# Kernel tuning notes

Measured on AMD Instinct MI355X. Metric: run time of the kernel, lower is better.

Reference implementation:

```python
import jax, jax.numpy as jnp
import numpy as np

DROPOUT_P = 0.5
SCALE = float(np.sqrt(128.0))  # sqrt(dk)


def setup_inputs() -> dict:
    key = jax.random.key(0)
    kq, kk, kv = jax.random.split(key, 3)
    B, H, S, D = 2, 16, 2048, 128
    return {
        "query": jax.random.normal(kq, (B, H, S, D), dtype=jnp.float32),
        "key": jax.random.normal(kk, (B, H, S, D), dtype=jnp.float32),
        "value": jax.random.normal(kv, (B, H, S, D), dtype=jnp.float32),
    }


def reference(query, key, value):
    # qk = Q @ K^T / scale  -> [B, H, Sq, Skv]
    scores = jnp.einsum("bhqd,bhkd->bhqk", query, key) / SCALE
    probs = jax.nn.softmax(scores, axis=-1)
    # dropout with inverted scaling (torch F.dropout semantics), fixed RNG key
    keep = jax.random.bernoulli(jax.random.key(42), 1.0 - DROPOUT_P, probs.shape)
    dropped = jnp.where(keep, probs / (1.0 - DROPOUT_P), 0.0)
    # output = dropped @ V  -> [B, H, Sq, Dv]
    return jnp.einsum("bhqk,bhkd->bhqd", dropped, value)
```

## Files before the change

### kernel.cpp

```cpp
#include <hip/hip_runtime.h>
#include <cstdint>

typedef __bf16 bf16x8 __attribute__((ext_vector_type(8)));
typedef __bf16 bf16x4 __attribute__((ext_vector_type(4)));
typedef __bf16 bf16x2 __attribute__((ext_vector_type(2)));
typedef float  f32x4  __attribute__((ext_vector_type(4)));

static constexpr int Hn = 16, Sn = 2048, Dn = 128;
static constexpr float SCALE_INV = 0.088388347648318447f;
static constexpr float M0 = 4.0f;

static constexpr size_t WS_KV = 8388608;
static constexpr size_t WS_NEED = 2 * WS_KV * 2;

__device__ __forceinline__ uint32_t rotl32(uint32_t v, int s) {
  return (v << s) | (v >> (32 - s));
}

__device__ __forceinline__ void tf2x32(uint32_t c0, uint32_t c1,
                                       uint32_t& o0, uint32_t& o1) {
  const uint32_t K1 = 42u, K2 = 0x1BD11BF0u;
  uint32_t x0 = c0, x1 = c1 + K1;
#define TF_R4(a,b,c,d) \
  x0 += x1; x1 = rotl32(x1,a) ^ x0; \
  x0 += x1; x1 = rotl32(x1,b) ^ x0; \
  x0 += x1; x1 = rotl32(x1,c) ^ x0; \
  x0 += x1; x1 = rotl32(x1,d) ^ x0;
  TF_R4(13,15,26,6)   x0 += K1;            x1 += K2 + 1u;
  TF_R4(17,29,16,24)  x0 += K2;            x1 += 2u;
  TF_R4(13,15,26,6)               x1 += K1 + 3u;
  TF_R4(17,29,16,24)  x0 += K1;            x1 += K2 + 4u;
  TF_R4(13,15,26,6)   x0 += K2;            x1 += 5u;
#undef TF_R4
  o0 = x0; o1 = x1;
}

__device__ __forceinline__ bf16x8 cvt8(f32x4 a, f32x4 b) {
  bf16x8 r;
  r[0] = (__bf16)a[0]; r[1] = (__bf16)a[1]; r[2] = (__bf16)a[2]; r[3] = (__bf16)a[3];
  r[4] = (__bf16)b[0]; r[5] = (__bf16)b[1]; r[6] = (__bf16)b[2]; r[7] = (__bf16)b[3];
  return r;
}

__global__ __launch_bounds__(256) void prep_cast(
    const float* __restrict__ K, const float* __restrict__ V,
    __bf16* __restrict__ Kb, __bf16* __restrict__ Vt)
{
  int bid = (int)blockIdx.x;
  if (bid < 4096) {
    size_t base = ((size_t)bid * 256 + threadIdx.x) * 8;
    f32x4 a = *(const f32x4*)(K + base);
    f32x4 b = *(const f32x4*)(K + base + 4);
    *(bf16x8*)(Kb + base) = cvt8(a, b);
  } else {
    bid -= 4096;
    int bh = bid >> 8, kvt = (bid >> 2) & 63, dt = bid & 3;
    __shared__ float tile[32][33];
    int r = (int)threadIdx.x >> 3, c4 = ((int)threadIdx.x & 7) * 4;
    const float* Vb = V + ((size_t)bh * Sn + (size_t)kvt * 32 + r) * Dn + dt * 32 + c4;
    f32x4 v = *(const f32x4*)Vb;
    tile[r][c4] = v[0]; tile[r][c4 + 1] = v[1];
    tile[r][c4 + 2] = v[2]; tile[r][c4 + 3] = v[3];
    __syncthreads();
    bf16x4 o;
    o[0] = (__bf16)tile[c4][r];     o[1] = (__bf16)tile[c4 + 1][r];
    o[2] = (__bf16)tile[c4 + 2][r]; o[3] = (__bf16)tile[c4 + 3][r];
    __bf16* dst = Vt + ((size_t)bh * Dn + dt * 32 + r) * Sn + (size_t)kvt * 32 + c4;
    *(bf16x4*)dst = o;
  }
}

__global__ __launch_bounds__(256, 4) void attn_bf16(
    const float* __restrict__ Qg, const __bf16* __restrict__ Kb,
    const __bf16* __restrict__ Vt, float* __restrict__ Og)
{
  const int tid  = threadIdx.x;
  const int lane = tid & 63;
  const int wv   = tid >> 6;
  const int g    = lane >> 4;
  const int qp   = lane & 15;

  const int bid = (int)blockIdx.x;
  const int qt  = bid & 31;
  const int bh  = bid >> 5;
  const uint32_t b_hi = (uint32_t)(bh >> 4) << 26;
  const uint32_t h_hi = (uint32_t)(bh & 15) << 22;

  const int q0 = qt * 64 + wv * 16;

  const size_t bhOff = (size_t)bh * Sn * Dn;
  const float*  Qb  = Qg + bhOff;
  const __bf16* Kbh = Kb + bhOff;
  const __bf16* Vbh = Vt + bhOff;
  float*        Ob  = Og + bhOff;

  bf16x8 qf[4];
  {
    const float* qrow = Qb + (size_t)(q0 + qp) * Dn + g * 8;
    #pragma unroll
    for (int c = 0; c < 4; ++c) {
      f32x4 a = *(const f32x4*)(qrow + c * 32);
      f32x4 b = *(const f32x4*)(qrow + c * 32 + 4);
      #pragma unroll
      for (int j = 0; j < 4; ++j) { a[j] *= SCALE_INV; b[j] *= SCALE_INV; }
      qf[c] = cvt8(a, b);
    }
  }

  f32x4 oacc[8];
  #pragma unroll
  for (int n = 0; n < 8; ++n) { f32x4 z = {0.f,0.f,0.f,0.f}; oacc[n] = z; }
  float l_run = 0.f;

  const uint32_t idx_base = b_hi + h_hi + ((uint32_t)(q0 + qp) << 11);

  for (int kv0 = 0; kv0 < Sn; kv0 += 32) {
    f32x4 st0 = {0.f,0.f,0.f,0.f}, st1 = {0.f,0.f,0.f,0.f};
    {
      const __bf16* kr0 = Kbh + (size_t)(kv0 + qp) * Dn + g * 8;
      const __bf16* kr1 = kr0 + (size_t)16 * Dn;
      #pragma unroll
      for (int c = 0; c < 4; ++c) {
        bf16x8 ka = *(const bf16x8*)(kr0 + c * 32);
        st0 = __builtin_amdgcn_mfma_f32_16x16x32_bf16(ka, qf[c], st0, 0, 0, 0);
        bf16x8 kb2 = *(const bf16x8*)(kr1 + c * 32);
        st1 = __builtin_amdgcn_mfma_f32_16x16x32_bf16(kb2, qf[c], st1, 0, 0, 0);
      }
    }

    float s[8] = { st0[0], st0[1], st0[2], st0[3], st1[0], st1[1], st1[2], st1[3] };
    uint32_t pk[4];
    float l_add = 0.f;
    #pragma unroll
    for (int m = 0; m < 4; ++m) {
      float p0 = __expf(s[2*m]     - M0);
      float p1 = __expf(s[2*m + 1] - M0);
      l_add += p0 + p1;
      uint32_t i0 = (uint32_t)(kv0 + (m >> 1) * 16 + g * 4 + ((2*m) & 3));
      uint32_t y0, y1, z0, z1;
      tf2x32(0u, idx_base + i0,      y0, y1);
      tf2x32(0u, idx_base + i0 + 1u, z0, z1);
      if ((int)(y0 ^ y1) < 0) p0 = 0.f;
      if ((int)(z0 ^ z1) < 0) p1 = 0.f;
      bf16x2 pr; pr[0] = (__bf16)p0; pr[1] = (__bf16)p1;
      union { bf16x2 h; uint32_t u; } cv; cv.h = pr;
      pk[m] = cv.u;
    }
    l_run += l_add;

    union { uint32_t u[4]; bf16x8 v; } pu;
    #pragma unroll
    for (int w = 0; w < 4; ++w) {
      int srcl = ((2 * (g & 1) + (w >> 1)) << 4) | qp;
      uint32_t lo = (uint32_t)__shfl((int)pk[w & 1],       srcl);
      uint32_t hi = (uint32_t)__shfl((int)pk[2 + (w & 1)], srcl);
      pu.u[w] = (g >= 2) ? hi : lo;
    }
    bf16x8 pa = pu.v;

    const __bf16* vcol = Vbh + (size_t)kv0 + (size_t)(g * 8);
    #pragma unroll
    for (int n = 0; n < 8; ++n) {
      bf16x8 vb = *(const bf16x8*)(vcol + (size_t)(n * 16 + qp) * Sn);
      oacc[n] = __builtin_amdgcn_mfma_f32_16x16x32_bf16(pa, vb, oacc[n], 0, 0, 0);
    }
  }

  l_run += __shfl_xor(l_run, 16);
  l_run += __shfl_xor(l_run, 32);
  float f = 2.0f / l_run;
  float fr[4];
  #pragma unroll
  for (int r = 0; r < 4; ++r) fr[r] = __shfl(f, g * 4 + r);

  float* orow = Ob + (size_t)q0 * Dn;
  #pragma unroll
  for (int n = 0; n < 8; ++n) {
    #pragma unroll
    for (int r = 0; r < 4; ++r) {
      orow[(size_t)(g * 4 + r) * Dn + n * 16 + qp] = oacc[n][r] * fr[r];
    }
  }
}

__global__ __launch_bounds__(256, 4) void attn_fwd_legacy(
    const float* __restrict__ Qg, const float* __restrict__ Kg,
    const float* __restrict__ Vg, float* __restrict__ Og)
{
  const int tid  = threadIdx.x;
  const int lane = tid & 63;
  const int wv   = tid >> 6;
  const int g    = lane >> 4;
  const int qp   = lane & 15;

  const int bid = (int)blockIdx.x;
  const int qt  = bid & 31;
  const int bh  = bid >> 5;
  const uint32_t b_hi = (uint32_t)(bh >> 4) << 26;
  const uint32_t h_hi = (uint32_t)(bh & 15) << 22;

  const int q0 = qt * 64 + wv * 16;
  __shared__ __bf16 Vts[128 * 40];

  const size_t bhOff = (size_t)bh * Sn * Dn;
  const float* Qb = Qg + bhOff;
  const float* Kb = Kg + bhOff;
  const float* Vb = Vg + bhOff;
  float*       Ob = Og + bhOff;

  bf16x8 qf[4];
  {
    const float* qrow = Qb + (size_t)(q0 + qp) * Dn + g * 8;
    #pragma unroll
    for (int c = 0; c < 4; ++c) {
      f32x4 a = *(const f32x4*)(qrow + c * 32);
      f32x4 b = *(const f32x4*)(qrow + c * 32 + 4);
      #pragma unroll
      for (int j = 0; j < 4; ++j) { a[j] *= SCALE_INV; b[j] *= SCALE_INV; }
      qf[c] = cvt8(a, b);
    }
  }

  f32x4 oacc[8];
  #pragma unroll
  for (int n = 0; n < 8; ++n) { f32x4 z = {0.f,0.f,0.f,0.f}; oacc[n] = z; }
  float m_run = -1e30f, l_run = 0.f;
  const int vr = (tid & 15) * 2;
  const int vc = (tid >> 4) * 8;
  const uint32_t idx_base = b_hi + h_hi + ((uint32_t)(q0 + qp) << 11);

  for (int kv0 = 0; kv0 < Sn; kv0 += 32) {
    const float* vp = Vb + (size_t)(kv0 + vr) * Dn + vc;
    f32x4 v0a = *(const f32x4*)(vp);
    f32x4 v0b = *(const f32x4*)(vp + 4);
    f32x4 v1a = *(const f32x4*)(vp + Dn);
    f32x4 v1b = *(const f32x4*)(vp + Dn + 4);

    f32x4 st0 = {0.f,0.f,0.f,0.f}, st1 = {0.f,0.f,0.f,0.f};
    {
      const float* krow0 = Kb + (size_t)(kv0 + qp) * Dn + g * 8;
      const float* krow1 = krow0 + (size_t)16 * Dn;
      #pragma unroll
      for (int c = 0; c < 4; ++c) {
        f32x4 a0 = *(const f32x4*)(krow0 + c * 32);
        f32x4 b0 = *(const f32x4*)(krow0 + c * 32 + 4);
        st0 = __builtin_amdgcn_mfma_f32_16x16x32_bf16(cvt8(a0, b0), qf[c], st0, 0, 0, 0);
        f32x4 a1 = *(const f32x4*)(krow1 + c * 32);
        f32x4 b1 = *(const f32x4*)(krow1 + c * 32 + 4);
        st1 = __builtin_amdgcn_mfma_f32_16x16x32_bf16(cvt8(a1, b1), qf[c], st1, 0, 0, 0);
      }
    }

    __syncthreads();
    #pragma unroll
    for (int i = 0; i < 8; ++i) {
      float x0 = (i < 4) ? v0a[i] : v0b[i - 4];
      float x1 = (i < 4) ? v1a[i] : v1b[i - 4];
      bf16x2 pr; pr[0] = (__bf16)x0; pr[1] = (__bf16)x1;
      *(bf16x2*)&Vts[(vc + i) * 40 + vr] = pr;
    }
    __syncthreads();

    float s[8] = { st0[0], st0[1], st0[2], st0[3], st1[0], st1[1], st1[2], st1[3] };
    float tmax = s[0];
    #pragma unroll
    for (int i = 1; i < 8; ++i) tmax = fmaxf(tmax, s[i]);
    tmax = fmaxf(tmax, __shfl_xor(tmax, 16));
    tmax = fmaxf(tmax, __shfl_xor(tmax, 32));
    float m_new = fmaxf(m_run, tmax);
    float alpha = __expf(m_run - m_new);

    float p[8], pd[8], psum = 0.f;
    #pragma unroll
    for (int i = 0; i < 8; ++i) {
      p[i] = __expf(s[i] - m_new);
      psum += p[i];
      uint32_t idx = idx_base + (uint32_t)(kv0 + (i >> 2) * 16 + g * 4 + (i & 3));
      uint32_t y0, y1;
      tf2x32(0u, idx, y0, y1);
      pd[i] = ((int)(y0 ^ y1) < 0) ? 0.f : p[i];
    }
    psum += __shfl_xor(psum, 16);
    psum += __shfl_xor(psum, 32);
    l_run = l_run * alpha + psum;
    m_run = m_new;

    float alr[4];
    #pragma unroll
    for (int r = 0; r < 4; ++r) alr[r] = __shfl(alpha, g * 4 + r);
    #pragma unroll
    for (int n = 0; n < 8; ++n) {
      f32x4 t = oacc[n];
      t[0] *= alr[0]; t[1] *= alr[1]; t[2] *= alr[2]; t[3] *= alr[3];
      oacc[n] = t;
    }

    bf16x8 pa;
    #pragma unroll
    for (int j = 0; j < 8; ++j) {
      int src = ((2 * (g & 1) + (j >> 2)) << 4) | qp;
      float v0 = __shfl(pd[j & 3],       src);
      float v1 = __shfl(pd[4 + (j & 3)], src);
      pa[j] = (__bf16)((g >= 2) ? v1 : v0);
    }

    #pragma unroll
    for (int n = 0; n < 8; ++n) {
      bf16x8 vb = *(const bf16x8*)&Vts[(n * 16 + qp) * 40 + g * 8];
      oacc[n] = __builtin_amdgcn_mfma_f32_16x16x32_bf16(pa, vb, oacc[n], 0, 0, 0);
    }
  }

  float f = 2.0f / l_run;
  float fr[4];
  #pragma unroll
  for (int r = 0; r < 4; ++r) fr[r] = __shfl(f, g * 4 + r);
  float* orow = Ob + (size_t)q0 * Dn;
  #pragma unroll
  for (int n = 0; n < 8; ++n) {
    #pragma unroll
    for (int r = 0; r < 4; ++r) {
      orow[(size_t)(g * 4 + r) * Dn + n * 16 + qp] = oacc[n][r] * fr[r];
    }
  }
}

extern "C" void kernel_launch(void* const* d_in, const int* in_sizes, int n_in,
                              void* d_out, int out_size, void* d_ws, size_t ws_size,
                              hipStream_t stream) {
  (void)in_sizes; (void)n_in; (void)out_size;
  const float* Q = (const float*)d_in[0];
  const float* K = (const float*)d_in[1];
  const float* V = (const float*)d_in[2];
  float* O = (float*)d_out;

  if (ws_size >= WS_NEED) {
    __bf16* Kb = (__bf16*)d_ws;
    __bf16* Vt = Kb + WS_KV;
    prep_cast<<<dim3(4096 + 8192), dim3(256), 0, stream>>>(K, V, Kb, Vt);
    attn_bf16<<<dim3(1024), dim3(256), 0, stream>>>(Q, Kb, Vt, O);
  } else {
    attn_fwd_legacy<<<dim3(1024), dim3(256), 0, stream>>>(Q, K, V, O);
  }
}
```

Before: 594.7 us.

## Precompute dropout mask bitfield and split KV loop across two blocks with combine

Moves the Threefry dropout RNG out of the attention inner loop into a prep kernel that writes a packed 32-bit keep mask per 32 keys. The attention kernel then reads one mask word per tile instead of hashing inline. The KV range is also split in half across 2048 blocks, with partial outputs and row sums written to workspace and merged by a new combine kernel. This trades inner-loop ALU work for extra mask traffic, partial-output traffic and an extra launch, and adds more parallelism.

```diff
diff --git a/kernel.cpp b/kernel.cpp
--- a/kernel.cpp
+++ b/kernel.cpp
@@ -10,8 +10,13 @@
 static constexpr float SCALE_INV = 0.088388347648318447f;
 static constexpr float M0 = 4.0f;
 
-static constexpr size_t WS_KV = 8388608;
-static constexpr size_t WS_NEED = 2 * WS_KV * 2;
+static constexpr size_t WS_KB_F  = 4194304;
+static constexpr size_t WS_VT_F  = 8388608;
+static constexpr size_t WS_U_F   = 12582912;
+static constexpr size_t WS_LP_F  = 29360128;
+static constexpr size_t WS_U_HALF = 8388608;
+static constexpr size_t NEED_B = 12582912ull * 4ull;
+static constexpr size_t NEED_A = (29360128ull + 131072ull) * 4ull;
 
 __device__ __forceinline__ uint32_t rotl32(uint32_t v, int s) {
   return (v << s) | (v >> (32 - s));
@@ -42,9 +47,10 @@
   return r;
 }
 
-__global__ __launch_bounds__(256) void prep_cast(
+__global__ __launch_bounds__(256) void prep_all(
     const float* __restrict__ K, const float* __restrict__ V,
-    __bf16* __restrict__ Kb, __bf16* __restrict__ Vt)
+    __bf16* __restrict__ Kb, __bf16* __restrict__ Vt,
+    uint32_t* __restrict__ mask)
 {
   int bid = (int)blockIdx.x;
   if (bid < 4096) {
@@ -52,7 +58,7 @@
     f32x4 a = *(const f32x4*)(K + base);
     f32x4 b = *(const f32x4*)(K + base + 4);
     *(bf16x8*)(Kb + base) = cvt8(a, b);
-  } else {
+  } else if (bid < 12288) {
     bid -= 4096;
     int bh = bid >> 8, kvt = (bid >> 2) & 63, dt = bid & 3;
     __shared__ float tile[32][33];
@@ -67,12 +73,26 @@
     o[2] = (__bf16)tile[c4 + 2][r]; o[3] = (__bf16)tile[c4 + 3][r];
     __bf16* dst = Vt + ((size_t)bh * Dn + dt * 32 + r) * Sn + (size_t)kvt * 32 + c4;
     *(bf16x4*)dst = o;
+  } else {
+    uint32_t widx = (uint32_t)(bid - 12288) * 256u + (uint32_t)threadIdx.x;
+    uint32_t base = widx << 5;
+    uint32_t w = 0;
+    #pragma unroll 8
+    for (int j = 0; j < 32; ++j) {
+      uint32_t y0, y1;
+      tf2x32(0u, base + (uint32_t)j, y0, y1);
+      uint32_t keep = (((y0 ^ y1) >> 31) ^ 1u);
+      w |= keep << j;
+    }
+    mask[widx] = w;
   }
 }
 
 __global__ __launch_bounds__(256, 4) void attn_bf16(
     const float* __restrict__ Qg, const __bf16* __restrict__ Kb,
-    const __bf16* __restrict__ Vt, float* __restrict__ Og)
+    const __bf16* __restrict__ Vt, const uint32_t* __restrict__ mask,
+    float* __restrict__ Og, float* __restrict__ U, float* __restrict__ LP,
+    int split)
 {
   const int tid  = threadIdx.x;
   const int lane = tid & 63;
@@ -80,11 +100,15 @@
   const int g    = lane >> 4;
   const int qp   = lane & 15;
 
-  const int bid = (int)blockIdx.x;
-  const int qt  = bid & 31;
-  const int bh  = bid >> 5;
+  const int bidl = (int)(blockIdx.x & 1023);
+  const int half = (int)(blockIdx.x >> 10);
+  const int qt  = bidl & 31;
+  const int bh  = bidl >> 5;
   const uint32_t b_hi = (uint32_t)(bh >> 4) << 26;
   const uint32_t h_hi = (uint32_t)(bh & 15) << 22;
+
+  const int kvlo = split ? half * 1024 : 0;
+  const int kvhi = kvlo + (split ? 1024 : 2048);
 
   const int q0 = qt * 64 + wv * 16;
 
@@ -113,8 +137,9 @@
   float l_run = 0.f;
 
   const uint32_t idx_base = b_hi + h_hi + ((uint32_t)(q0 + qp) << 11);
-
-  for (int kv0 = 0; kv0 < Sn; kv0 += 32) {
+  const uint32_t* mrow = mask + (idx_base >> 5);
+
+  for (int kv0 = kvlo; kv0 < kvhi; kv0 += 32) {
     f32x4 st0 = {0.f,0.f,0.f,0.f}, st1 = {0.f,0.f,0.f,0.f};
     {
       const __bf16* kr0 = Kbh + (size_t)(kv0 + qp) * Dn + g * 8;
@@ -128,6 +153,7 @@
       }
     }
 
+    const uint32_t mw = mrow[kv0 >> 5];
     float s[8] = { st0[0], st0[1], st0[2], st0[3], st1[0], st1[1], st1[2], st1[3] };
     uint32_t pk[4];
     float l_add = 0.f;
@@ -136,12 +162,9 @@
       float p0 = __expf(s[2*m]     - M0);
       float p1 = __expf(s[2*m + 1] - M0);
       l_add += p0 + p1;
-      uint32_t i0 = (uint32_t)(kv0 + (m >> 1) * 16 + g * 4 + ((2*m) & 3));
-      uint32_t y0, y1, z0, z1;
-      tf2x32(0u, idx_base + i0,      y0, y1);
-      tf2x32(0u, idx_base + i0 + 1u, z0, z1);
-      if ((int)(y0 ^ y1) < 0) p0 = 0.f;
-      if ((int)(z0 ^ z1) < 0) p1 = 0.f;
+      const int b0 = (m >> 1) * 16 + g * 4 + ((2*m) & 3);
+      if (!((mw >> b0) & 1u))       p0 = 0.f;
+      if (!((mw >> (b0 + 1)) & 1u)) p1 = 0.f;
       bf16x2 pr; pr[0] = (__bf16)p0; pr[1] = (__bf16)p1;
       union { bf16x2 h; uint32_t u; } cv; cv.h = pr;
       pk[m] = cv.u;
@@ -168,19 +191,49 @@
 
   l_run += __shfl_xor(l_run, 16);
   l_run += __shfl_xor(l_run, 32);
-  float f = 2.0f / l_run;
-  float fr[4];
+
+  if (!split) {
+    float f = 2.0f / l_run;
+    float fr[4];
+    #pragma unroll
+    for (int r = 0; r < 4; ++r) fr[r] = __shfl(f, g * 4 + r);
+    float* orow = Ob + (size_t)q0 * Dn;
+    #pragma unroll
+    for (int n = 0; n < 8; ++n) {
+      #pragma unroll
+      for (int r = 0; r < 4; ++r) {
+        orow[(size_t)(g * 4 + r) * Dn + n * 16 + qp] = oacc[n][r] * fr[r];
+      }
+    }
+  } else {
+    float* Urow = U + (size_t)half * WS_U_HALF + bhOff + (size_t)q0 * Dn;
+    #pragma unroll
+    for (int n = 0; n < 8; ++n) {
+      #pragma unroll
+      for (int r = 0; r < 4; ++r) {
+        Urow[(size_t)(g * 4 + r) * Dn + n * 16 + qp] = oacc[n][r];
+      }
+    }
+    if (lane < 16) {
+      LP[(size_t)half * 65536 + (size_t)bh * Sn + (size_t)(q0 + qp)] = l_run;
+    }
+  }
+}
+
+__global__ __launch_bounds__(256) void attn_combine(
+    const float* __restrict__ U, const float* __restrict__ LP,
+    float* __restrict__ Og)
+{
+  int idx = (int)blockIdx.x * 256 + (int)threadIdx.x;
+  size_t row = (size_t)(idx >> 5);
+  int c4 = (idx & 31) * 4;
+  float inv = 2.0f / (LP[row] + LP[65536 + row]);
+  const f32x4 u1 = *(const f32x4*)(U + row * Dn + c4);
+  const f32x4 u2 = *(const f32x4*)(U + WS_U_HALF + row * Dn + c4);
+  f32x4 o;
   #pragma unroll
-  for (int r = 0; r < 4; ++r) fr[r] = __shfl(f, g * 4 + r);
-
-  float* orow = Ob + (size_t)q0 * Dn;
-  #pragma unroll
-  for (int n = 0; n < 8; ++n) {
-    #pragma unroll
-    for (int r = 0; r < 4; ++r) {
-      orow[(size_t)(g * 4 + r) * Dn + n * 16 + qp] = oacc[n][r] * fr[r];
-    }
-  }
+  for (int j = 0; j < 4; ++j) o[j] = (u1[j] + u2[j]) * inv;
+  *(f32x4*)(Og + row * Dn + c4) = o;
 }
 
 __global__ __launch_bounds__(256, 4) void attn_fwd_legacy(
@@ -334,11 +387,20 @@
   const float* V = (const float*)d_in[2];
   float* O = (float*)d_out;
 
-  if (ws_size >= WS_NEED) {
-    __bf16* Kb = (__bf16*)d_ws;
-    __bf16* Vt = Kb + WS_KV;
-    prep_cast<<<dim3(4096 + 8192), dim3(256), 0, stream>>>(K, V, Kb, Vt);
-    attn_bf16<<<dim3(1024), dim3(256), 0, stream>>>(Q, Kb, Vt, O);
+  if (ws_size >= NEED_B) {
+    float*    wsf  = (float*)d_ws;
+    uint32_t* mask = (uint32_t*)d_ws;
+    __bf16*   Kb   = (__bf16*)(wsf + WS_KB_F);
+    __bf16*   Vt   = (__bf16*)(wsf + WS_VT_F);
+    prep_all<<<dim3(4096 + 8192 + 16384), dim3(256), 0, stream>>>(K, V, Kb, Vt, mask);
+    if (ws_size >= NEED_A) {
+      float* U  = wsf + WS_U_F;
+      float* LP = wsf + WS_LP_F;
+      attn_bf16<<<dim3(2048), dim3(256), 0, stream>>>(Q, Kb, Vt, mask, O, U, LP, 1);
+      attn_combine<<<dim3(8192), dim3(256), 0, stream>>>(U, LP, O);
+    } else {
+      attn_bf16<<<dim3(1024), dim3(256), 0, stream>>>(Q, Kb, Vt, mask, O, nullptr, nullptr, 0);
+    }
   } else {
     attn_fwd_legacy<<<dim3(1024), dim3(256), 0, stream>>>(Q, K, V, O);
   }
```

Result: slower. 914.6 us (+53.8%).
